# Optimization experiments

Hardware: AMD Instinct MI355X
Metric: run time of the kernel (lower is better)

## Reference

```python
import jax, jax.numpy as jnp
import numpy as np

B, C, C2, E = 4, 1024, 1024, 1024
D = 1024          # context_size (d_q = d_kv)
NH = 16           # module's n_heads arg -> actual head_dim after the quirky view
G = D // NH       # effective number of head groups = 64


def setup_inputs() -> dict:
    key = jax.random.key(0)
    ks = jax.random.split(key, 6)
    s = 0.02
    return {
        "x1": jax.random.normal(ks[0], (B, C, E), dtype=jnp.float32),
        "x2": jax.random.normal(ks[1], (B, C2, E), dtype=jnp.float32),
        "W_q": jax.random.normal(ks[2], (E, D), dtype=jnp.float32) * s,
        "W_k": jax.random.normal(ks[3], (E, D), dtype=jnp.float32) * s,
        "W_v": jax.random.normal(ks[4], (E, D), dtype=jnp.float32) * s,
        "W_o": jax.random.normal(ks[5], (D, D), dtype=jnp.float32) * s,
    }


def _split_heads(t):
    # (B, S, D) -> view (B, S, G, NH) -> transpose(1,2) -> (B, G, S, NH)
    b, s, _ = t.shape
    return jnp.transpose(t.reshape(b, s, G, NH), (0, 2, 1, 3))


def reference(x1, x2, W_q, W_k, W_v, W_o):
    Q = _split_heads(x1 @ W_q)   # (B, G, C, NH)
    K = _split_heads(x2 @ W_k)   # (B, G, C2, NH)
    V = _split_heads(x2 @ W_v)   # (B, G, C2, NH)
    scale = 1.0 / jnp.sqrt(jnp.asarray(NH, dtype=Q.dtype))
    scores = jnp.einsum("bgqh,bgkh->bgqk", Q, K) * scale  # (B, G, C, C2)
    w = jax.nn.softmax(scores, axis=-1)
    out = jnp.einsum("bgqk,bgkh->bgqh", w, V)             # (B, G, C, NH)
    out = jnp.transpose(out, (0, 2, 1, 3)).reshape(B, C, D)
    return out @ W_o  # dropout p=0 -> identity
```

## Files before the change

kernel.cpp:

```cpp
#include <hip/hip_runtime.h>


typedef _Float16 f16x8 __attribute__((ext_vector_type(8)));
typedef _Float16 f16x4 __attribute__((ext_vector_type(4)));
typedef _Float16 f16x2 __attribute__((ext_vector_type(2)));
typedef float    f32x4 __attribute__((ext_vector_type(4)));
typedef float    f32x16 __attribute__((ext_vector_type(16)));

#define GLOAD_LDS16(gp, lp)                                              \
    __builtin_amdgcn_global_load_lds(                                    \
        (const __attribute__((address_space(1))) void*)(gp),             \
        (__attribute__((address_space(3))) void*)(lp), 16, 0, 0)

static __device__ __forceinline__ f16x8 pack8f(const float* p) {
    f16x2 a = __builtin_bit_cast(f16x2, __builtin_amdgcn_cvt_pkrtz(p[0], p[1]));
    f16x2 b = __builtin_bit_cast(f16x2, __builtin_amdgcn_cvt_pkrtz(p[2], p[3]));
    f16x2 c = __builtin_bit_cast(f16x2, __builtin_amdgcn_cvt_pkrtz(p[4], p[5]));
    f16x2 d = __builtin_bit_cast(f16x2, __builtin_amdgcn_cvt_pkrtz(p[6], p[7]));
    f16x8 r;
    r[0] = a[0]; r[1] = a[1]; r[2] = b[0]; r[3] = b[1];
    r[4] = c[0]; r[5] = c[1]; r[6] = d[0]; r[7] = d[1];
    return r;
}

__global__ __launch_bounds__(256) void prep_kernel(
        const float* __restrict__ x1, const float* __restrict__ x2,
        const float* __restrict__ W0, const float* __restrict__ W1,
        const float* __restrict__ W2, const float* __restrict__ W3,
        _Float16* __restrict__ y1, _Float16* __restrict__ y2,
        _Float16* __restrict__ T0, _Float16* __restrict__ T1,
        _Float16* __restrict__ T2, _Float16* __restrict__ T3) {
    int bx = blockIdx.x, tid = threadIdx.x;
    if (bx < 8192) {
        int i = bx * 256 + tid;
        const float* x = (i < 1048576) ? x1 : x2;
        _Float16* y = (i < 1048576) ? y1 : y2;
        int j = i & 1048575;
        float4 v = ((const float4*)x)[j];
        f16x4 h = { (_Float16)v.x, (_Float16)v.y, (_Float16)v.z, (_Float16)v.w };
        ((f16x4*)y)[j] = h;
    } else {
        int z = (bx - 8192) >> 10;
        const float* W = (z == 0) ? W0 : (z == 1) ? W1 : (z == 2) ? W2 : W3;
        _Float16* WT = (z == 0) ? T0 : (z == 1) ? T1 : (z == 2) ? T2 : T3;
        int t = (bx - 8192) & 1023;
        int c0 = (t & 31) * 32, r0 = (t >> 5) * 32;
        __shared__ float tile[32][33];
        int tx = tid & 31, ty = tid >> 5;
#pragma unroll
        for (int i = 0; i < 32; i += 8)
            tile[ty + i][tx] = W[(r0 + ty + i) * 1024 + (c0 + tx)];
        __syncthreads();
#pragma unroll
        for (int i = 0; i < 32; i += 8)
            WT[(c0 + ty + i) * 1024 + (r0 + tx)] = (_Float16)tile[tx][ty + i];
    }
}

template <bool OUTF32>
static __device__ __forceinline__ void gemm_body(const _Float16* __restrict__ Atile,
                                                 const _Float16* __restrict__ BTtile,
                                                 void* __restrict__ Ctile,
                                                 _Float16* As, _Float16* Bs) {
    const int tid = threadIdx.x, lane = tid & 63, wave = tid >> 6;
    const int wm = wave >> 1, wn = wave & 1;
    const int col = lane & 15, quad = lane >> 4;

    f32x4 acc[4][4];
#pragma unroll
    for (int i = 0; i < 4; i++)
#pragma unroll
        for (int j = 0; j < 4; j++) acc[i][j] = (f32x4){0.f, 0.f, 0.f, 0.f};

    const int srow = wave * 8 + (lane >> 3);
    const int sch = (lane & 7) * 8;
    const _Float16* Ag = Atile + (size_t)srow * 1024 + sch;
    const _Float16* Bg = BTtile + (size_t)srow * 1024 + sch;
    _Float16* Asl = As + wave * 512;
    _Float16* Bsl = Bs + wave * 512;

    for (int kt = 0; kt < 16; kt++) {
        __syncthreads();
#pragma unroll
        for (int c = 0; c < 4; c++) {
            GLOAD_LDS16(Ag + (size_t)(c * 32) * 1024 + kt * 64, Asl + c * 2048);
            GLOAD_LDS16(Bg + (size_t)(c * 32) * 1024 + kt * 64, Bsl + c * 2048);
        }
        __syncthreads();
#pragma unroll
        for (int ki = 0; ki < 2; ki++) {
            f16x8 af[4], bf[4];
#pragma unroll
            for (int i = 0; i < 4; i++)
                af[i] = *(const f16x8*)(As + (wm * 64 + i * 16 + col) * 64 + ki * 32 + quad * 8);
#pragma unroll
            for (int j = 0; j < 4; j++)
                bf[j] = *(const f16x8*)(Bs + (wn * 64 + j * 16 + col) * 64 + ki * 32 + quad * 8);
#pragma unroll
            for (int i = 0; i < 4; i++)
#pragma unroll
                for (int j = 0; j < 4; j++)
                    acc[i][j] = __builtin_amdgcn_mfma_f32_16x16x32_f16(af[i], bf[j], acc[i][j], 0, 0, 0);
        }
    }

#pragma unroll
    for (int i = 0; i < 4; i++)
#pragma unroll
        for (int ii = 0; ii < 4; ii++) {
            int row = wm * 64 + i * 16 + quad * 4 + ii;
#pragma unroll
            for (int j = 0; j < 4; j++) {
                int cc = wn * 64 + j * 16 + col;
                if (OUTF32) ((float*)Ctile)[(size_t)row * 1024 + cc] = acc[i][j][ii];
                else ((_Float16*)Ctile)[(size_t)row * 1024 + cc] = (_Float16)acc[i][j][ii];
            }
        }
}

__global__ __launch_bounds__(256, 3) void gemm_qkv_kernel(
        const _Float16* __restrict__ x1h, const _Float16* __restrict__ x2h,
        const _Float16* __restrict__ WqT, const _Float16* __restrict__ WkvT,
        _Float16* __restrict__ Qh, _Float16* __restrict__ Kh, _Float16* __restrict__ Vh) {
    __shared__ _Float16 As[128 * 64], Bs[128 * 64];
    int gx = blockIdx.x;
    const _Float16 *A, *BT;
    _Float16* C;
    int m0, n0;
    if (gx < 256) {
        m0 = (gx >> 3) * 128; n0 = (gx & 7) * 128;
        A = x1h; BT = WqT + (size_t)n0 * 1024; C = Qh + n0;
    } else {
        int idx = gx - 256;
        m0 = (idx >> 4) * 128;
        int nb = idx & 15;
        n0 = nb * 128;
        A = x2h; BT = WkvT + (size_t)n0 * 1024;
        C = (nb < 8) ? (Kh + n0) : (Vh + (n0 - 1024));
    }
    gemm_body<false>(A + (size_t)m0 * 1024, BT, (void*)(C + (size_t)m0 * 1024), As, Bs);
}

__global__ __launch_bounds__(256, 3) void gemm_wo_kernel(const _Float16* __restrict__ Ah,
                                                         const _Float16* __restrict__ WoT,
                                                         float* __restrict__ out) {
    __shared__ _Float16 As[128 * 64], Bs[128 * 64];
    int m0 = blockIdx.y * 128, n0 = blockIdx.x * 128;
    gemm_body<true>(Ah + (size_t)m0 * 1024, WoT + (size_t)n0 * 1024,
                    (void*)(out + (size_t)m0 * 1024 + n0), As, Bs);
}

__global__ __launch_bounds__(256, 8) void attn_kernel(const _Float16* __restrict__ Qh,
                                                      const _Float16* __restrict__ Kh,
                                                      const _Float16* __restrict__ Vh,
                                                      _Float16* __restrict__ Ah) {
    int pair = blockIdx.y;
    int b = pair >> 6, g = pair & 63;
    __shared__ _Float16 KA[4096];
    __shared__ _Float16 VA[4096];
    __shared__ _Float16 ones[8];

    const _Float16* Kg = Kh + (size_t)(b * 1024) * 1024 + g * 16;
    const _Float16* Vg = Vh + (size_t)(b * 1024) * 1024 + g * 16;
    int tid = threadIdx.x;
    if (tid < 8) ones[tid] = (_Float16)1.f;

    int lane = tid & 63, wave = tid >> 6;
    int n = lane & 31, h5 = lane >> 5;
    int q0 = blockIdx.x * 128 + wave * 32;

    f16x8 qf;
    {
        f16x8 t = *(const f16x8*)(Qh + (size_t)(b * 1024 + q0 + n) * 1024 + g * 16 + h5 * 8);
#pragma unroll
        for (int j = 0; j < 8; j++) qf[j] = (_Float16)((float)t[j] * 0.360673760f);
    }

    f32x16 acc = {0.f, 0.f, 0.f, 0.f, 0.f, 0.f, 0.f, 0.f,
                  0.f, 0.f, 0.f, 0.f, 0.f, 0.f, 0.f, 0.f};
    const f32x16 zero16 = acc;
    const _Float16* vbase = (n < 16) ? (VA + (n + 16 * h5) * 8) : ones;
    const int vstep = (n < 16) ? 256 : 0;

    for (int c = 0; c < 4; c++) {
        if (c) __syncthreads();
#pragma unroll
        for (int it = 0; it < 2; it++) {
            int row = it * 128 + (tid >> 1);
            int part = tid & 1;
            int pm = (row & 19) | ((row & 4) << 1) | ((row & 8) >> 1);
            *(uint4*)(KA + (((row >> 5) * 64) + pm + 32 * part) * 8) =
                *(const uint4*)(Kg + (size_t)(c * 256 + row) * 1024 + part * 8);
        }
#pragma unroll
        for (int it = 0; it < 2; it++) {
            int row = it * 128 + (tid >> 1);
            int part = tid & 1;
            f16x8 v = *(const f16x8*)(Vg + (size_t)(c * 256 + row) * 1024 + part * 8);
            int base = (row >> 4) * 256 + ((row >> 3) & 1) * 128 + part * 64 + (row & 7);
#pragma unroll
            for (int j = 0; j < 8; j++) VA[base + j * 8] = v[j];
        }
        __syncthreads();

#pragma unroll 2
        for (int t = 0; t < 8; t++) {
            f16x8 ak = *(const f16x8*)(KA + (t * 64 + lane) * 8);
            f32x16 s = __builtin_amdgcn_mfma_f32_32x32x16_f16(ak, qf, zero16, 0, 0, 0);
            float p[16];
#pragma unroll
            for (int i = 0; i < 16; i++) p[i] = __builtin_amdgcn_exp2f(s[i]);
            f16x8 pb0 = pack8f(p);
            f16x8 pb1 = pack8f(p + 8);
            f16x8 av0 = *(const f16x8*)(vbase + (2 * t) * vstep);
            f16x8 av1 = *(const f16x8*)(vbase + (2 * t + 1) * vstep);
            acc = __builtin_amdgcn_mfma_f32_32x32x16_f16(av0, pb0, acc, 0, 0, 0);
            acc = __builtin_amdgcn_mfma_f32_32x32x16_f16(av1, pb1, acc, 0, 0, 0);
        }
    }

    float rl = 1.0f / acc[8];
    f16x4 o0, o1;
#pragma unroll
    for (int i = 0; i < 4; i++) o0[i] = (_Float16)(acc[i] * rl);
#pragma unroll
    for (int i = 0; i < 4; i++) o1[i] = (_Float16)(acc[4 + i] * rl);
    _Float16* ob = Ah + (size_t)(b * 1024 + q0 + n) * 1024 + g * 16 + h5 * 4;
    *(f16x4*)(ob) = o0;
    *(f16x4*)(ob + 8) = o1;
}

extern "C" void kernel_launch(void* const* d_in, const int* in_sizes, int n_in,
                              void* d_out, int out_size, void* d_ws, size_t ws_size,
                              hipStream_t stream) {
    const float* x1 = (const float*)d_in[0];
    const float* x2 = (const float*)d_in[1];
    const float* Wq = (const float*)d_in[2];
    const float* Wk = (const float*)d_in[3];
    const float* Wv = (const float*)d_in[4];
    const float* Wo = (const float*)d_in[5];

    char* ws = (char*)d_ws;
    const size_t MB = 1u << 20;
    if (ws_size < 56 * MB) return;

    _Float16* x1h = (_Float16*)(ws + 0 * MB);
    _Float16* x2h = (_Float16*)(ws + 8 * MB);
    _Float16* WqT = (_Float16*)(ws + 16 * MB);
    _Float16* WkT = (_Float16*)(ws + 18 * MB);
    _Float16* WvT = (_Float16*)(ws + 20 * MB);
    _Float16* WoT = (_Float16*)(ws + 22 * MB);
    _Float16* Qh  = (_Float16*)(ws + 24 * MB);
    _Float16* Kh  = (_Float16*)(ws + 32 * MB);
    _Float16* Vh  = (_Float16*)(ws + 40 * MB);
    _Float16* Ah  = (_Float16*)(ws + 48 * MB);

    prep_kernel<<<12288, 256, 0, stream>>>(x1, x2, Wq, Wk, Wv, Wo,
                                           x1h, x2h, WqT, WkT, WvT, WoT);

    gemm_qkv_kernel<<<768, 256, 0, stream>>>(x1h, x2h, WqT, WkT, Qh, Kh, Vh);

    attn_kernel<<<dim3(8, 256), 256, 0, stream>>>(Qh, Kh, Vh, Ah);

    gemm_wo_kernel<<<dim3(8, 32), 256, 0, stream>>>(Ah, WoT, (float*)d_out);
}
```

Measured before the change: 203.5 us.

## Halve Wo GEMM M-tile and shrink attention K/V LDS chunks

The output-projection GEMM is templated on M-tile size and now uses 64-row tiles, giving 512 blocks instead of 256 and raising the occupancy hint to fill more CUs. The attention kernel stages K/V in 128-row chunks instead of 256, halving its LDS footprint to allow more resident blocks. V transposition now writes packed f16x2 pairs instead of scalar halves, with only half the threads loading V. The trade-off is more barriers per attention block and less operand reuse per Wo GEMM tile.

```diff
diff --git a/kernel.cpp b/kernel.cpp
--- a/kernel.cpp
+++ b/kernel.cpp
@@ -57,18 +57,19 @@
     }
 }
 
-template <bool OUTF32>
+template <int MT, bool OUTF32>
 static __device__ __forceinline__ void gemm_body(const _Float16* __restrict__ Atile,
                                                  const _Float16* __restrict__ BTtile,
                                                  void* __restrict__ Ctile,
                                                  _Float16* As, _Float16* Bs) {
+    constexpr int AF = MT / 32;
     const int tid = threadIdx.x, lane = tid & 63, wave = tid >> 6;
     const int wm = wave >> 1, wn = wave & 1;
     const int col = lane & 15, quad = lane >> 4;
 
-    f32x4 acc[4][4];
-#pragma unroll
-    for (int i = 0; i < 4; i++)
+    f32x4 acc[AF][4];
+#pragma unroll
+    for (int i = 0; i < AF; i++)
 #pragma unroll
         for (int j = 0; j < 4; j++) acc[i][j] = (f32x4){0.f, 0.f, 0.f, 0.f};
 
@@ -82,22 +83,23 @@
     for (int kt = 0; kt < 16; kt++) {
         __syncthreads();
 #pragma unroll
-        for (int c = 0; c < 4; c++) {
+        for (int c = 0; c < AF; c++)
             GLOAD_LDS16(Ag + (size_t)(c * 32) * 1024 + kt * 64, Asl + c * 2048);
+#pragma unroll
+        for (int c = 0; c < 4; c++)
             GLOAD_LDS16(Bg + (size_t)(c * 32) * 1024 + kt * 64, Bsl + c * 2048);
-        }
         __syncthreads();
 #pragma unroll
         for (int ki = 0; ki < 2; ki++) {
-            f16x8 af[4], bf[4];
-#pragma unroll
-            for (int i = 0; i < 4; i++)
-                af[i] = *(const f16x8*)(As + (wm * 64 + i * 16 + col) * 64 + ki * 32 + quad * 8);
+            f16x8 af[AF], bf[4];
+#pragma unroll
+            for (int i = 0; i < AF; i++)
+                af[i] = *(const f16x8*)(As + (wm * (MT / 2) + i * 16 + col) * 64 + ki * 32 + quad * 8);
 #pragma unroll
             for (int j = 0; j < 4; j++)
                 bf[j] = *(const f16x8*)(Bs + (wn * 64 + j * 16 + col) * 64 + ki * 32 + quad * 8);
 #pragma unroll
-            for (int i = 0; i < 4; i++)
+            for (int i = 0; i < AF; i++)
 #pragma unroll
                 for (int j = 0; j < 4; j++)
                     acc[i][j] = __builtin_amdgcn_mfma_f32_16x16x32_f16(af[i], bf[j], acc[i][j], 0, 0, 0);
@@ -105,10 +107,10 @@
     }
 
 #pragma unroll
-    for (int i = 0; i < 4; i++)
+    for (int i = 0; i < AF; i++)
 #pragma unroll
         for (int ii = 0; ii < 4; ii++) {
-            int row = wm * 64 + i * 16 + quad * 4 + ii;
+            int row = wm * (MT / 2) + i * 16 + quad * 4 + ii;
 #pragma unroll
             for (int j = 0; j < 4; j++) {
                 int cc = wn * 64 + j * 16 + col;
@@ -138,16 +140,17 @@
         A = x2h; BT = WkvT + (size_t)n0 * 1024;
         C = (nb < 8) ? (Kh + n0) : (Vh + (n0 - 1024));
     }
-    gemm_body<false>(A + (size_t)m0 * 1024, BT, (void*)(C + (size_t)m0 * 1024), As, Bs);
-}
-
-__global__ __launch_bounds__(256, 3) void gemm_wo_kernel(const _Float16* __restrict__ Ah,
+    gemm_body<128, false>(A + (size_t)m0 * 1024, BT, (void*)(C + (size_t)m0 * 1024), As, Bs);
+}
+
+__global__ __launch_bounds__(256, 4) void gemm_wo_kernel(const _Float16* __restrict__ Ah,
                                                          const _Float16* __restrict__ WoT,
                                                          float* __restrict__ out) {
-    __shared__ _Float16 As[128 * 64], Bs[128 * 64];
-    int m0 = blockIdx.y * 128, n0 = blockIdx.x * 128;
-    gemm_body<true>(Ah + (size_t)m0 * 1024, WoT + (size_t)n0 * 1024,
-                    (void*)(out + (size_t)m0 * 1024 + n0), As, Bs);
+    __shared__ _Float16 As[64 * 64], Bs[128 * 64];
+    int gx = blockIdx.x;
+    int m0 = (gx >> 3) * 64, n0 = (gx & 7) * 128;
+    gemm_body<64, true>(Ah + (size_t)m0 * 1024, WoT + (size_t)n0 * 1024,
+                        (void*)(out + (size_t)m0 * 1024 + n0), As, Bs);
 }
 
 __global__ __launch_bounds__(256, 8) void attn_kernel(const _Float16* __restrict__ Qh,
@@ -156,8 +159,8 @@
                                                       _Float16* __restrict__ Ah) {
     int pair = blockIdx.y;
     int b = pair >> 6, g = pair & 63;
-    __shared__ _Float16 KA[4096];
-    __shared__ _Float16 VA[4096];
+    __shared__ _Float16 KA[2048];
+    __shared__ _Float16 VA[2048];
     __shared__ _Float16 ones[8];
 
     const _Float16* Kg = Kh + (size_t)(b * 1024) * 1024 + g * 16;
@@ -182,29 +185,29 @@
     const _Float16* vbase = (n < 16) ? (VA + (n + 16 * h5) * 8) : ones;
     const int vstep = (n < 16) ? 256 : 0;
 
-    for (int c = 0; c < 4; c++) {
+    const int krow = tid >> 1, kpart = tid & 1;
+    const int kpm = (krow & 19) | ((krow & 4) << 1) | ((krow & 8) >> 1);
+    const int kdst = (((krow >> 5) * 64) + kpm + 32 * kpart) * 8;
+    const int vk0 = (tid >> 1) * 2 & 127, vpart = tid & 1;
+    const int vbase_w = (vk0 >> 4) * 256 + ((vk0 >> 3) & 1) * 128 + vpart * 64 + (vk0 & 7);
+
+    for (int c = 0; c < 8; c++) {
         if (c) __syncthreads();
-#pragma unroll
-        for (int it = 0; it < 2; it++) {
-            int row = it * 128 + (tid >> 1);
-            int part = tid & 1;
-            int pm = (row & 19) | ((row & 4) << 1) | ((row & 8) >> 1);
-            *(uint4*)(KA + (((row >> 5) * 64) + pm + 32 * part) * 8) =
-                *(const uint4*)(Kg + (size_t)(c * 256 + row) * 1024 + part * 8);
-        }
-#pragma unroll
-        for (int it = 0; it < 2; it++) {
-            int row = it * 128 + (tid >> 1);
-            int part = tid & 1;
-            f16x8 v = *(const f16x8*)(Vg + (size_t)(c * 256 + row) * 1024 + part * 8);
-            int base = (row >> 4) * 256 + ((row >> 3) & 1) * 128 + part * 64 + (row & 7);
-#pragma unroll
-            for (int j = 0; j < 8; j++) VA[base + j * 8] = v[j];
-        }
-        __syncthreads();
-
-#pragma unroll 2
-        for (int t = 0; t < 8; t++) {
+        *(uint4*)(KA + kdst) =
+            *(const uint4*)(Kg + (size_t)(c * 128 + krow) * 1024 + kpart * 8);
+        if (tid < 128) {
+            f16x8 v0 = *(const f16x8*)(Vg + (size_t)(c * 128 + vk0) * 1024 + vpart * 8);
+            f16x8 v1 = *(const f16x8*)(Vg + (size_t)(c * 128 + vk0 + 1) * 1024 + vpart * 8);
+#pragma unroll
+            for (int j = 0; j < 8; j++) {
+                f16x2 pr; pr[0] = v0[j]; pr[1] = v1[j];
+                *(f16x2*)(VA + vbase_w + j * 8) = pr;
+            }
+        }
+        __syncthreads();
+
+#pragma unroll
+        for (int t = 0; t < 4; t++) {
             f16x8 ak = *(const f16x8*)(KA + (t * 64 + lane) * 8);
             f32x16 s = __builtin_amdgcn_mfma_f32_32x32x16_f16(ak, qf, zero16, 0, 0, 0);
             float p[16];
@@ -262,5 +265,5 @@
 
     attn_kernel<<<dim3(8, 256), 256, 0, stream>>>(Qh, Kh, Vh, Ah);
 
-    gemm_wo_kernel<<<dim3(8, 32), 256, 0, stream>>>(Ah, WoT, (float*)d_out);
-}
+    gemm_wo_kernel<<<512, 256, 0, stream>>>(Ah, WoT, (float*)d_out);
+}
```

Result: faster. 194.8 us (-4.3%).
